# Kernel tuning notes

Hardware: AMD Instinct MI355X
Metric: run time of the kernel (lower is better)

Reference implementation:

```python
import jax, jax.numpy as jnp
import numpy as np

ROPE_BASE = 10000.0

def apply_rope(x):
    # x: [B, S, H, Dh]  (rotate-half / NeoX convention)
    B, S, H, Dh = x.shape
    inv_freq = 1.0 / (ROPE_BASE ** (jnp.arange(0, Dh, 2, dtype=jnp.float32) / Dh))  # [Dh/2]
    ang = jnp.arange(S, dtype=jnp.float32)[:, None] * inv_freq[None, :]             # [S, Dh/2]
    cos = jnp.cos(ang)[None, :, None, :].astype(x.dtype)  # [1,S,1,Dh/2]
    sin = jnp.sin(ang)[None, :, None, :].astype(x.dtype)
    x1, x2 = jnp.split(x, 2, axis=-1)
    return jnp.concatenate([x1 * cos - x2 * sin, x1 * sin + x2 * cos], axis=-1)

def setup_inputs() -> dict:
    key = jax.random.key(0)
    k1, k2, k3 = jax.random.split(key, 3)
    B, S, D = 2, 2048, 1024
    x = jax.random.normal(k1, (B, S, D), dtype=jnp.float32)
    attn_mask = jnp.ones((B, S), dtype=bool)
    qkv_w = jax.random.normal(k2, (D, 3 * D), dtype=jnp.float32) * (1.0 / np.sqrt(D))
    out_w = jax.random.normal(k3, (D, D), dtype=jnp.float32) * (1.0 / np.sqrt(D))
    return {"x": x, "qkv_w": qkv_w, "out_w": out_w, "attn_mask": attn_mask, "is_causal": 1}

def reference(x, qkv_w, out_w, attn_mask, is_causal):
    B, S, D = x.shape
    H = 16
    Dh = D // H
    qkv = x @ qkv_w                                  # [B,S,3D]
    q, k, v = jnp.split(qkv, 3, axis=-1)
    q = apply_rope(q.reshape(B, S, H, Dh))           # [B,S,H,Dh]
    k = apply_rope(k.reshape(B, S, H, Dh))
    v = v.reshape(B, S, H, Dh)
    scale = 1.0 / np.sqrt(Dh)
    att = jnp.einsum('bqhd,bkhd->bhqk', q, k) * scale  # [B,H,S,S]
    if is_causal:
        mask = jnp.tril(jnp.ones((S, S), dtype=bool))[None, None]
    else:
        mask = attn_mask[:, None, None, :]             # [B,1,1,S]
    att = jnp.where(mask, att, jnp.finfo(att.dtype).min)
    p = jax.nn.softmax(att, axis=-1)
    y = jnp.einsum('bhqk,bkhd->bqhd', p, v).reshape(B, S, D)
    return y @ out_w
```

## Files before the change

### kernel.cpp

```cpp
#include <hip/hip_runtime.h>
#include <hip/hip_bf16.h>

#define BB 2
#define SS 2048
#define DD 1024
#define HH 16
#define N3 3072

typedef __attribute__((ext_vector_type(8))) short bf16x8;
typedef __attribute__((ext_vector_type(4))) float f32x4;
typedef __attribute__((ext_vector_type(2))) unsigned int u32x2;

__device__ __forceinline__ float b2f(unsigned short u) {
    return __uint_as_float(((unsigned int)u) << 16);
}
__device__ __forceinline__ unsigned short f2b(float f) {
    unsigned int x = __float_as_uint(f);
    x += 0x7fffu + ((x >> 16) & 1u);
    return (unsigned short)(x >> 16);
}
__device__ __forceinline__ unsigned int pack2bf(float a, float b) {
    __hip_bfloat162 h = __float22bfloat162_rn(make_float2(a, b));
    return *(unsigned int*)&h;
}
__device__ __forceinline__ void storeC(float* p, float v) { *p = v; }
__device__ __forceinline__ void storeC(unsigned short* p, float v) { *p = f2b(v); }

__device__ __forceinline__ void gload_lds16(const void* g, void* l) {
    __builtin_amdgcn_global_load_lds(
        (__attribute__((address_space(1))) void*)g,
        (__attribute__((address_space(3))) void*)l, 16, 0, 0);
}

__global__ __launch_bounds__(256) void sincos_tab(float2* __restrict__ tab) {
    int i = blockIdx.x * 256 + threadIdx.x;
    int t = i & 31;
    int s = i >> 5;
    float inv = powf(10000.0f, -(float)t * (1.0f / 32.0f));
    float sn, c;
    sincosf((float)s * inv, &sn, &c);
    tab[i] = make_float2(c, sn);
}

__global__ __launch_bounds__(256) void cast_f32_bf16(
    const float* __restrict__ src, unsigned short* __restrict__ dst)
{
    int i = (blockIdx.x * 256 + threadIdx.x) * 4;
    float4 f = *(const float4*)(src + i);
    uint2 o;
    o.x = pack2bf(f.x, f.y);
    o.y = pack2bf(f.z, f.w);
    *(uint2*)(dst + i) = o;
}

__global__ __launch_bounds__(256) void cast_transpose(
    const float* __restrict__ src, unsigned short* __restrict__ dst,
    int R, int C)
{
    __shared__ unsigned short tile[64][66];
    const int t = threadIdx.x;
    const int c0 = blockIdx.x * 64, r0 = blockIdx.y * 64;
    const int lr = t >> 4;
    const int lc = (t & 15) * 4;
    #pragma unroll
    for (int i = 0; i < 4; ++i) {
        float4 f = *(const float4*)(src + (size_t)(r0 + lr + i * 16) * C + c0 + lc);
        tile[lr + i * 16][lc + 0] = f2b(f.x);
        tile[lr + i * 16][lc + 1] = f2b(f.y);
        tile[lr + i * 16][lc + 2] = f2b(f.z);
        tile[lr + i * 16][lc + 3] = f2b(f.w);
    }
    __syncthreads();
    #pragma unroll
    for (int i = 0; i < 4; ++i) {
        const int wr = lr + i * 16;
        ushort4 o;
        o.x = tile[lc + 0][wr];
        o.y = tile[lc + 1][wr];
        o.z = tile[lc + 2][wr];
        o.w = tile[lc + 3][wr];
        *(ushort4*)(dst + (size_t)(c0 + wr) * R + r0 + lc) = o;
    }
}

template <typename OutT, int TN>
__global__ __launch_bounds__(256) void gemm_mfma(
    const unsigned short* __restrict__ A,
    const unsigned short* __restrict__ Bt,
    OutT* __restrict__ C,
    int M, int N, int K)
{
    constexpr int NI = TN / 32;
    constexpr int NB = TN / 64;
    __shared__ unsigned short Al[128 * 32];
    __shared__ unsigned short Bl[TN * 32];
    const int tid  = threadIdx.x;
    const int wave = tid >> 6;
    const int lane = tid & 63;
    const int quad = lane >> 4;
    const int l16  = lane & 15;
    const int m0 = blockIdx.y * 128;
    const int n0 = blockIdx.x * TN;
    const int wm = (wave >> 1) * 64;
    const int wn = (wave & 1) * (TN / 2);

    const int srowA = wave * 32 + (lane >> 2);
    const int srowB = wave * (16 * NB) + (lane >> 2);
    const int scol  = (lane & 3) * 8;
    const unsigned short* gA = A  + (size_t)(m0 + srowA) * K + scol;
    const unsigned short* gB = Bt + (size_t)(n0 + srowB) * K + scol;

    f32x4 acc[4][NI];
    #pragma unroll
    for (int mi = 0; mi < 4; ++mi)
        #pragma unroll
        for (int ni = 0; ni < NI; ++ni)
            acc[mi][ni] = (f32x4){0.f, 0.f, 0.f, 0.f};

    for (int k0 = 0; k0 < K; k0 += 32) {
        __syncthreads();
        #pragma unroll
        for (int i = 0; i < 2; ++i)
            gload_lds16(gA + (size_t)i * 16 * K + k0, Al + (wave * 2 + i) * 512);
        #pragma unroll
        for (int i = 0; i < NB; ++i)
            gload_lds16(gB + (size_t)i * 16 * K + k0, Bl + (wave * NB + i) * 512);
        __syncthreads();

        bf16x8 af[4], bfr[NI];
        #pragma unroll
        for (int mi = 0; mi < 4; ++mi)
            af[mi] = *(const bf16x8*)&Al[(wm + mi * 16 + l16) * 32 + quad * 8];
        #pragma unroll
        for (int ni = 0; ni < NI; ++ni)
            bfr[ni] = *(const bf16x8*)&Bl[(wn + ni * 16 + l16) * 32 + quad * 8];
        #pragma unroll
        for (int mi = 0; mi < 4; ++mi)
            #pragma unroll
            for (int ni = 0; ni < NI; ++ni)
                acc[mi][ni] = __builtin_amdgcn_mfma_f32_16x16x32_bf16(
                    af[mi], bfr[ni], acc[mi][ni], 0, 0, 0);
    }

    #pragma unroll
    for (int mi = 0; mi < 4; ++mi) {
        #pragma unroll
        for (int r = 0; r < 4; ++r) {
            const size_t base = (size_t)(m0 + wm + mi * 16 + quad * 4 + r) * N + n0 + wn;
            #pragma unroll
            for (int ni = 0; ni < NI; ++ni)
                storeC(&C[base + ni * 16 + l16], acc[mi][ni][r]);
        }
    }
}

__global__ __launch_bounds__(256) void rope_split(
    const unsigned short* __restrict__ qkv,
    const float2* __restrict__ tab,
    unsigned short* __restrict__ qo,
    unsigned short* __restrict__ ko,
    unsigned short* __restrict__ vt)
{
    __shared__ unsigned short Vtile[64][72];

    const float SC = 0.18033688011112042f;
    const int s0 = blockIdx.x * 64;
    const int h  = blockIdx.y;
    const int b  = blockIdx.z;
    const int tid = threadIdx.x;
    const int sl = tid >> 2;
    const int qu = tid & 3;
    const size_t bh = (size_t)b * HH + h;

    const unsigned short* row = qkv + (size_t)(b * SS + s0 + sl) * N3 + h * 64;

    uint4 a0 = *(const uint4*)(row + qu * 8);
    uint4 a1 = *(const uint4*)(row + 32 + qu * 8);
    uint4 b0 = *(const uint4*)(row + DD + qu * 8);
    uint4 b1 = *(const uint4*)(row + DD + 32 + qu * 8);
    uint4 c0 = *(const uint4*)(row + 2 * DD + qu * 8);
    uint4 c1 = *(const uint4*)(row + 2 * DD + 32 + qu * 8);

    float2 cs[8];
    {
        const float4* tp = (const float4*)(tab + (size_t)(s0 + sl) * 32 + qu * 8);
        #pragma unroll
        for (int i = 0; i < 4; ++i) {
            float4 f = tp[i];
            cs[2 * i]     = make_float2(f.x, f.y);
            cs[2 * i + 1] = make_float2(f.z, f.w);
        }
    }

    const unsigned short* pa0 = (const unsigned short*)&a0;
    const unsigned short* pa1 = (const unsigned short*)&a1;
    const unsigned short* pb0 = (const unsigned short*)&b0;
    const unsigned short* pb1 = (const unsigned short*)&b1;
    const unsigned short* pc0 = (const unsigned short*)&c0;
    const unsigned short* pc1 = (const unsigned short*)&c1;

    unsigned short oq1[8], oq2[8], ok1[8], ok2[8];
    #pragma unroll
    for (int j = 0; j < 8; ++j) {
        float c = cs[j].x, sn = cs[j].y;
        float q1 = b2f(pa0[j]), q2 = b2f(pa1[j]);
        float k1 = b2f(pb0[j]), k2 = b2f(pb1[j]);
        oq1[j] = f2b((q1 * c - q2 * sn) * SC);
        oq2[j] = f2b((q1 * sn + q2 * c) * SC);
        ok1[j] = f2b(k1 * c - k2 * sn);
        ok2[j] = f2b(k1 * sn + k2 * c);
        Vtile[qu * 8 + j][sl]      = pc0[j];
        Vtile[32 + qu * 8 + j][sl] = pc1[j];
    }
    const size_t qoff = (bh * SS + s0 + sl) * 64;
    *(uint4*)(qo + qoff + qu * 8)      = *(const uint4*)oq1;
    *(uint4*)(qo + qoff + 32 + qu * 8) = *(const uint4*)oq2;
    *(uint4*)(ko + qoff + qu * 8)      = *(const uint4*)ok1;
    *(uint4*)(ko + qoff + 32 + qu * 8) = *(const uint4*)ok2;

    __syncthreads();

    const int dr = tid >> 2;
    const int ch = tid & 3;
    uint4 t0 = *(const uint4*)&Vtile[dr][ch * 16];
    uint4 t1 = *(const uint4*)&Vtile[dr][ch * 16 + 8];
    unsigned short* vrow = vt + (bh * 64 + dr) * SS + s0 + ch * 16;
    *(uint4*)vrow       = t0;
    *(uint4*)(vrow + 8) = t1;
}

__device__ __forceinline__ void attn_step(
    const unsigned short* __restrict__ Kb,
    const unsigned short* __restrict__ Vb,
    const bf16x8 qf0, const bf16x8 qf1, const bf16x8 onesf,
    f32x4 O[4], f32x4& l_acc,
    bool diag, const unsigned char* mrow,
    int kt, int quad, int l16, int csw, int qg)
{
    f32x4 Sf[4];
    #pragma unroll
    for (int st = 0; st < 4; ++st) {
        const unsigned short* kr = &Kb[(st * 16 + l16) * 64];
        bf16x8 kf0 = *(const bf16x8*)(kr + csw * 8);
        bf16x8 kf1 = *(const bf16x8*)(kr + (csw ^ 4) * 8);
        f32x4 s = (f32x4){0.f, 0.f, 0.f, 0.f};
        s = __builtin_amdgcn_mfma_f32_16x16x32_bf16(kf0, qf0, s, 0, 0, 0);
        s = __builtin_amdgcn_mfma_f32_16x16x32_bf16(kf1, qf1, s, 0, 0, 0);
        Sf[st] = s;
    }

    if (diag) {
        #pragma unroll
        for (int st = 0; st < 4; ++st) {
            const int kb0 = kt * 64 + st * 16 + quad * 4;
            #pragma unroll
            for (int r = 0; r < 4; ++r)
                if (kb0 + r > qg) Sf[st][r] = -1e30f;
        }
    } else if (mrow) {
        #pragma unroll
        for (int st = 0; st < 4; ++st) {
            uchar4 mv = *(const uchar4*)(mrow + st * 16 + quad * 4);
            if (!mv.x) Sf[st][0] = -1e30f;
            if (!mv.y) Sf[st][1] = -1e30f;
            if (!mv.z) Sf[st][2] = -1e30f;
            if (!mv.w) Sf[st][3] = -1e30f;
        }
    }

    #pragma unroll
    for (int st = 0; st < 4; ++st)
        #pragma unroll
        for (int r = 0; r < 4; ++r)
            Sf[st][r] = exp2f(Sf[st][r]);

    unsigned int W[4][2];
    #pragma unroll
    for (int st = 0; st < 4; ++st) {
        W[st][0] = pack2bf(Sf[st][0], Sf[st][1]);
        W[st][1] = pack2bf(Sf[st][2], Sf[st][3]);
    }

    unsigned int pw0[4], pw1[4];
    #pragma unroll
    for (int j = 0; j < 2; ++j) {
        u32x2 s1 = __builtin_amdgcn_permlane32_swap(W[0][j], W[1][j], false, false);
        u32x2 s2 = __builtin_amdgcn_permlane16_swap(s1.x, s1.y, false, false);
        pw0[j]     = s2.x;
        pw0[j + 2] = s2.y;
        u32x2 t1 = __builtin_amdgcn_permlane32_swap(W[2][j], W[3][j], false, false);
        u32x2 t2 = __builtin_amdgcn_permlane16_swap(t1.x, t1.y, false, false);
        pw1[j]     = t2.x;
        pw1[j + 2] = t2.y;
    }
    bf16x8 pf0 = *(const bf16x8*)pw0;
    bf16x8 pf1 = *(const bf16x8*)pw1;

    l_acc = __builtin_amdgcn_mfma_f32_16x16x32_bf16(onesf, pf0, l_acc, 0, 0, 0);
    l_acc = __builtin_amdgcn_mfma_f32_16x16x32_bf16(onesf, pf1, l_acc, 0, 0, 0);

    #pragma unroll
    for (int st = 0; st < 4; ++st) {
        const unsigned short* vr = &Vb[(st * 16 + l16) * 64];
        bf16x8 vf0 = *(const bf16x8*)(vr + csw * 8);
        bf16x8 vf1 = *(const bf16x8*)(vr + (csw ^ 4) * 8);
        O[st] = __builtin_amdgcn_mfma_f32_16x16x32_bf16(vf0, pf0, O[st], 0, 0, 0);
        O[st] = __builtin_amdgcn_mfma_f32_16x16x32_bf16(vf1, pf1, O[st], 0, 0, 0);
    }
}

__global__ __launch_bounds__(128) void flash_attn(
    const unsigned short* __restrict__ q,
    const unsigned short* __restrict__ k,
    const unsigned short* __restrict__ vt,
    unsigned short* __restrict__ y,
    const int* __restrict__ is_causal,
    const unsigned char* __restrict__ attn_mask)
{
    __shared__ unsigned short Kl[64 * 64];
    __shared__ unsigned short Vl[64 * 64];

    const int bid  = blockIdx.x;
    const int work = ((bid & 7) << 8) | (bid >> 3);
    const int bhi  = work >> 6;
    const int j    = 63 - (work & 63);
    const int b = bhi >> 4;
    const int h = bhi & 15;

    const int tid  = threadIdx.x;
    const int wave = tid >> 6;
    const int lane = tid & 63;
    const int quad = lane >> 4;
    const int l16  = lane & 15;

    const size_t bh = (size_t)b * HH + h;
    const bool causal = (is_causal[0] != 0);
    const int NT = SS / 64;
    const int tW = j >> 1;
    const int ntrips = causal ? (tW + 1) : NT;

    const unsigned short* qrow = q + (bh * SS + j * 32 + wave * 16 + l16) * 64;
    const bf16x8 qf0 = *(const bf16x8*)(qrow + quad * 8);
    const bf16x8 qf1 = *(const bf16x8*)(qrow + 32 + quad * 8);

    bf16x8 onesf;
    #pragma unroll
    for (int i = 0; i < 8; ++i) onesf[i] = (short)0x3F80;

    const unsigned short* kbase  = k  + bh * SS * 64;
    const unsigned short* vtbase = vt + bh * 64 * SS;

    const int Rl  = lane >> 3;
    const int cph = lane & 7;
    const int csw = quad ^ (l16 & 7);

    f32x4 O[4];
    #pragma unroll
    for (int st = 0; st < 4; ++st) O[st] = (f32x4){0.f, 0.f, 0.f, 0.f};
    f32x4 l_acc = (f32x4){0.f, 0.f, 0.f, 0.f};

    const int qg = j * 32 + wave * 16 + l16;

    auto stage = [&](int kt) {
        #pragma unroll
        for (int i = 0; i < 4; ++i) {
            const int jj = wave * 4 + i;
            const int R  = jj * 8 + Rl;
            const int cl = cph ^ (R & 7);
            gload_lds16(kbase + ((size_t)(kt * 64 + R) * 64 + cl * 8),
                        &Kl[jj * 512]);
            gload_lds16(vtbase + ((size_t)R * SS + kt * 64 + cl * 8),
                        &Vl[jj * 512]);
        }
    };

    for (int kt = 0; kt < ntrips; ++kt) {
        __syncthreads();
        stage(kt);
        __syncthreads();

        const unsigned char* mrow = causal ? nullptr
                                           : (attn_mask + (size_t)b * SS + kt * 64);
        attn_step(Kl, Vl, qf0, qf1, onesf, O, l_acc,
                  causal && kt == tW, mrow, kt, quad, l16, csw, qg);
    }

    const float inv = 1.0f / l_acc[0];
    unsigned short* yrow = y + ((size_t)b * SS + qg) * DD + h * 64;
    #pragma unroll
    for (int st = 0; st < 4; ++st) {
        uint2 o;
        o.x = pack2bf(O[st][0] * inv, O[st][1] * inv);
        o.y = pack2bf(O[st][2] * inv, O[st][3] * inv);
        *(uint2*)(yrow + st * 16 + quad * 4) = o;
    }
}

extern "C" void kernel_launch(void* const* d_in, const int* in_sizes, int n_in,
                              void* d_out, int out_size, void* d_ws, size_t ws_size,
                              hipStream_t stream) {
    const float* x      = (const float*)d_in[0];
    const float* qkv_w  = (const float*)d_in[1];
    const float* out_w  = (const float*)d_in[2];
    const unsigned char* mask = (const unsigned char*)d_in[3];
    const int*   is_c   = (const int*)d_in[4];
    float* out = (float*)d_out;

    unsigned short* xb  = (unsigned short*)d_ws;
    unsigned short* w1t = xb  + (size_t)4096 * 1024;
    unsigned short* w2t = w1t + (size_t)3072 * 1024;
    unsigned short* qkv = w2t + (size_t)1024 * 1024;
    unsigned short* qb  = qkv + (size_t)4096 * 3072;
    unsigned short* kb  = qb  + (size_t)BB * HH * SS * 64;
    unsigned short* vt  = kb  + (size_t)BB * HH * SS * 64;
    float2* tab = (float2*)(vt + (size_t)BB * HH * SS * 64);
    unsigned short* yb = xb;

    sincos_tab<<<(SS * 32) / 256, 256, 0, stream>>>(tab);
    cast_f32_bf16<<<(4096 * 1024) / 1024, 256, 0, stream>>>(x, xb);
    cast_transpose<<<dim3(N3 / 64, DD / 64), 256, 0, stream>>>(qkv_w, w1t, DD, N3);
    cast_transpose<<<dim3(DD / 64, DD / 64), 256, 0, stream>>>(out_w, w2t, DD, DD);

    gemm_mfma<unsigned short, 128><<<dim3(N3 / 128, 4096 / 128), 256, 0, stream>>>(
        xb, w1t, qkv, 4096, N3, DD);

    rope_split<<<dim3(SS / 64, HH, BB), 256, 0, stream>>>(qkv, tab, qb, kb, vt);

    flash_attn<<<dim3(BB * HH * (SS / 32)), 128, 0, stream>>>(qb, kb, vt, yb, is_c, mask);

    gemm_mfma<float, 64><<<dim3(DD / 64, 4096 / 128), 256, 0, stream>>>(
        yb, w2t, out, 4096, DD, DD);
}
```

Before: 217.7 us.

## Load K/V fragments directly from global in single-wave flash attention blocks

```diff
diff --git a/kernel.cpp b/kernel.cpp
--- a/kernel.cpp
+++ b/kernel.cpp
@@ -229,87 +229,7 @@
     *(uint4*)(vrow + 8) = t1;
 }
 
-__device__ __forceinline__ void attn_step(
-    const unsigned short* __restrict__ Kb,
-    const unsigned short* __restrict__ Vb,
-    const bf16x8 qf0, const bf16x8 qf1, const bf16x8 onesf,
-    f32x4 O[4], f32x4& l_acc,
-    bool diag, const unsigned char* mrow,
-    int kt, int quad, int l16, int csw, int qg)
-{
-    f32x4 Sf[4];
-    #pragma unroll
-    for (int st = 0; st < 4; ++st) {
-        const unsigned short* kr = &Kb[(st * 16 + l16) * 64];
-        bf16x8 kf0 = *(const bf16x8*)(kr + csw * 8);
-        bf16x8 kf1 = *(const bf16x8*)(kr + (csw ^ 4) * 8);
-        f32x4 s = (f32x4){0.f, 0.f, 0.f, 0.f};
-        s = __builtin_amdgcn_mfma_f32_16x16x32_bf16(kf0, qf0, s, 0, 0, 0);
-        s = __builtin_amdgcn_mfma_f32_16x16x32_bf16(kf1, qf1, s, 0, 0, 0);
-        Sf[st] = s;
-    }
-
-    if (diag) {
-        #pragma unroll
-        for (int st = 0; st < 4; ++st) {
-            const int kb0 = kt * 64 + st * 16 + quad * 4;
-            #pragma unroll
-            for (int r = 0; r < 4; ++r)
-                if (kb0 + r > qg) Sf[st][r] = -1e30f;
-        }
-    } else if (mrow) {
-        #pragma unroll
-        for (int st = 0; st < 4; ++st) {
-            uchar4 mv = *(const uchar4*)(mrow + st * 16 + quad * 4);
-            if (!mv.x) Sf[st][0] = -1e30f;
-            if (!mv.y) Sf[st][1] = -1e30f;
-            if (!mv.z) Sf[st][2] = -1e30f;
-            if (!mv.w) Sf[st][3] = -1e30f;
-        }
-    }
-
-    #pragma unroll
-    for (int st = 0; st < 4; ++st)
-        #pragma unroll
-        for (int r = 0; r < 4; ++r)
-            Sf[st][r] = exp2f(Sf[st][r]);
-
-    unsigned int W[4][2];
-    #pragma unroll
-    for (int st = 0; st < 4; ++st) {
-        W[st][0] = pack2bf(Sf[st][0], Sf[st][1]);
-        W[st][1] = pack2bf(Sf[st][2], Sf[st][3]);
-    }
-
-    unsigned int pw0[4], pw1[4];
-    #pragma unroll
-    for (int j = 0; j < 2; ++j) {
-        u32x2 s1 = __builtin_amdgcn_permlane32_swap(W[0][j], W[1][j], false, false);
-        u32x2 s2 = __builtin_amdgcn_permlane16_swap(s1.x, s1.y, false, false);
-        pw0[j]     = s2.x;
-        pw0[j + 2] = s2.y;
-        u32x2 t1 = __builtin_amdgcn_permlane32_swap(W[2][j], W[3][j], false, false);
-        u32x2 t2 = __builtin_amdgcn_permlane16_swap(t1.x, t1.y, false, false);
-        pw1[j]     = t2.x;
-        pw1[j + 2] = t2.y;
-    }
-    bf16x8 pf0 = *(const bf16x8*)pw0;
-    bf16x8 pf1 = *(const bf16x8*)pw1;
-
-    l_acc = __builtin_amdgcn_mfma_f32_16x16x32_bf16(onesf, pf0, l_acc, 0, 0, 0);
-    l_acc = __builtin_amdgcn_mfma_f32_16x16x32_bf16(onesf, pf1, l_acc, 0, 0, 0);
-
-    #pragma unroll
-    for (int st = 0; st < 4; ++st) {
-        const unsigned short* vr = &Vb[(st * 16 + l16) * 64];
-        bf16x8 vf0 = *(const bf16x8*)(vr + csw * 8);
-        bf16x8 vf1 = *(const bf16x8*)(vr + (csw ^ 4) * 8);
-        O[st] = __builtin_amdgcn_mfma_f32_16x16x32_bf16(vf0, pf0, O[st], 0, 0, 0);
-        O[st] = __builtin_amdgcn_mfma_f32_16x16x32_bf16(vf1, pf1, O[st], 0, 0, 0);
-    }
-}
-
-__global__ __launch_bounds__(128) void flash_attn(
+__global__ __launch_bounds__(64, 4) void flash_attn(
     const unsigned short* __restrict__ q,
     const unsigned short* __restrict__ k,
     const unsigned short* __restrict__ vt,
@@ -317,29 +237,26 @@
     const int* __restrict__ is_causal,
     const unsigned char* __restrict__ attn_mask)
 {
-    __shared__ unsigned short Kl[64 * 64];
-    __shared__ unsigned short Vl[64 * 64];
-
     const int bid  = blockIdx.x;
-    const int work = ((bid & 7) << 8) | (bid >> 3);
-    const int bhi  = work >> 6;
-    const int j    = 63 - (work & 63);
+    const int work = ((bid & 7) << 9) | (bid >> 3);
+    const int bhi  = work >> 7;
+    const int slot = work & 127;
+    const int tile = 31 - (slot >> 2);
+    const int frag = slot & 3;
     const int b = bhi >> 4;
     const int h = bhi & 15;
 
-    const int tid  = threadIdx.x;
-    const int wave = tid >> 6;
-    const int lane = tid & 63;
+    const int lane = threadIdx.x;
     const int quad = lane >> 4;
     const int l16  = lane & 15;
 
     const size_t bh = (size_t)b * HH + h;
     const bool causal = (is_causal[0] != 0);
     const int NT = SS / 64;
-    const int tW = j >> 1;
-    const int ntrips = causal ? (tW + 1) : NT;
-
-    const unsigned short* qrow = q + (bh * SS + j * 32 + wave * 16 + l16) * 64;
+    const int ntrips = causal ? (tile + 1) : NT;
+
+    const int qg = tile * 64 + frag * 16 + l16;
+    const unsigned short* qrow = q + (bh * SS + qg) * 64;
     const bf16x8 qf0 = *(const bf16x8*)(qrow + quad * 8);
     const bf16x8 qf1 = *(const bf16x8*)(qrow + 32 + quad * 8);
 
@@ -347,42 +264,95 @@
     #pragma unroll
     for (int i = 0; i < 8; ++i) onesf[i] = (short)0x3F80;
 
-    const unsigned short* kbase  = k  + bh * SS * 64;
-    const unsigned short* vtbase = vt + bh * 64 * SS;
-
-    const int Rl  = lane >> 3;
-    const int cph = lane & 7;
-    const int csw = quad ^ (l16 & 7);
+    const unsigned short* kbase  = k  + bh * SS * 64 + (size_t)l16 * 64 + quad * 8;
+    const unsigned short* vtbase = vt + bh * 64 * SS + (size_t)l16 * SS + quad * 8;
 
     f32x4 O[4];
     #pragma unroll
     for (int st = 0; st < 4; ++st) O[st] = (f32x4){0.f, 0.f, 0.f, 0.f};
     f32x4 l_acc = (f32x4){0.f, 0.f, 0.f, 0.f};
 
-    const int qg = j * 32 + wave * 16 + l16;
-
-    auto stage = [&](int kt) {
-        #pragma unroll
-        for (int i = 0; i < 4; ++i) {
-            const int jj = wave * 4 + i;
-            const int R  = jj * 8 + Rl;
-            const int cl = cph ^ (R & 7);
-            gload_lds16(kbase + ((size_t)(kt * 64 + R) * 64 + cl * 8),
-                        &Kl[jj * 512]);
-            gload_lds16(vtbase + ((size_t)R * SS + kt * 64 + cl * 8),
-                        &Vl[jj * 512]);
-        }
-    };
-
     for (int kt = 0; kt < ntrips; ++kt) {
-        __syncthreads();
-        stage(kt);
-        __syncthreads();
-
-        const unsigned char* mrow = causal ? nullptr
-                                           : (attn_mask + (size_t)b * SS + kt * 64);
-        attn_step(Kl, Vl, qf0, qf1, onesf, O, l_acc,
-                  causal && kt == tW, mrow, kt, quad, l16, csw, qg);
+        f32x4 Sf[4];
+        {
+            bf16x8 kf[4][2];
+            #pragma unroll
+            for (int st = 0; st < 4; ++st) {
+                const unsigned short* kr = kbase + (size_t)(kt * 64 + st * 16) * 64;
+                kf[st][0] = *(const bf16x8*)kr;
+                kf[st][1] = *(const bf16x8*)(kr + 32);
+            }
+            #pragma unroll
+            for (int st = 0; st < 4; ++st) {
+                f32x4 s = (f32x4){0.f, 0.f, 0.f, 0.f};
+                s = __builtin_amdgcn_mfma_f32_16x16x32_bf16(kf[st][0], qf0, s, 0, 0, 0);
+                s = __builtin_amdgcn_mfma_f32_16x16x32_bf16(kf[st][1], qf1, s, 0, 0, 0);
+                Sf[st] = s;
+            }
+        }
+
+        bf16x8 vf[4][2];
+        #pragma unroll
+        for (int st = 0; st < 4; ++st) {
+            const unsigned short* vr = vtbase + (size_t)(st * 16) * SS + kt * 64;
+            vf[st][0] = *(const bf16x8*)vr;
+            vf[st][1] = *(const bf16x8*)(vr + 32);
+        }
+
+        if (causal && kt == tile) {
+            #pragma unroll
+            for (int st = 0; st < 4; ++st) {
+                const int kb0 = kt * 64 + st * 16 + quad * 4;
+                #pragma unroll
+                for (int r = 0; r < 4; ++r)
+                    if (kb0 + r > qg) Sf[st][r] = -1e30f;
+            }
+        } else if (!causal) {
+            const unsigned char* mrow = attn_mask + (size_t)b * SS + kt * 64;
+            #pragma unroll
+            for (int st = 0; st < 4; ++st) {
+                uchar4 mv = *(const uchar4*)(mrow + st * 16 + quad * 4);
+                if (!mv.x) Sf[st][0] = -1e30f;
+                if (!mv.y) Sf[st][1] = -1e30f;
+                if (!mv.z) Sf[st][2] = -1e30f;
+                if (!mv.w) Sf[st][3] = -1e30f;
+            }
+        }
+
+        #pragma unroll
+        for (int st = 0; st < 4; ++st)
+            #pragma unroll
+            for (int r = 0; r < 4; ++r)
+                Sf[st][r] = exp2f(Sf[st][r]);
+
+        unsigned int W[4][2];
+        #pragma unroll
+        for (int st = 0; st < 4; ++st) {
+            W[st][0] = pack2bf(Sf[st][0], Sf[st][1]);
+            W[st][1] = pack2bf(Sf[st][2], Sf[st][3]);
+        }
+        unsigned int pw0[4], pw1[4];
+        #pragma unroll
+        for (int j = 0; j < 2; ++j) {
+            u32x2 s1 = __builtin_amdgcn_permlane32_swap(W[0][j], W[1][j], false, false);
+            u32x2 s2 = __builtin_amdgcn_permlane16_swap(s1.x, s1.y, false, false);
+            pw0[j]     = s2.x;
+            pw0[j + 2] = s2.y;
+            u32x2 t1 = __builtin_amdgcn_permlane32_swap(W[2][j], W[3][j], false, false);
+            u32x2 t2 = __builtin_amdgcn_permlane16_swap(t1.x, t1.y, false, false);
+            pw1[j]     = t2.x;
+            pw1[j + 2] = t2.y;
+        }
+        bf16x8 pf0 = *(const bf16x8*)pw0;
+        bf16x8 pf1 = *(const bf16x8*)pw1;
+
+        l_acc = __builtin_amdgcn_mfma_f32_16x16x32_bf16(onesf, pf0, l_acc, 0, 0, 0);
+        l_acc = __builtin_amdgcn_mfma_f32_16x16x32_bf16(onesf, pf1, l_acc, 0, 0, 0);
+        #pragma unroll
+        for (int st = 0; st < 4; ++st) {
+            O[st] = __builtin_amdgcn_mfma_f32_16x16x32_bf16(vf[st][0], pf0, O[st], 0, 0, 0);
+            O[st] = __builtin_amdgcn_mfma_f32_16x16x32_bf16(vf[st][1], pf1, O[st], 0, 0, 0);
+        }
     }
 
     const float inv = 1.0f / l_acc[0];
@@ -426,7 +396,7 @@
 
     rope_split<<<dim3(SS / 64, HH, BB), 256, 0, stream>>>(qkv, tab, qb, kb, vt);
 
-    flash_attn<<<dim3(BB * HH * (SS / 32)), 128, 0, stream>>>(qb, kb, vt, yb, is_c, mask);
+    flash_attn<<<dim3(BB * HH * 128), 64, 0, stream>>>(qb, kb, vt, yb, is_c, mask);
 
     gemm_mfma<float, 64><<<dim3(DD / 64, 4096 / 128), 256, 0, stream>>>(
         yb, w2t, out, 4096, DD, DD);
```

New measurement: 301.5 us. +38.5%, slower.
